# Kernel optimization log

Measured on AMD Instinct MI355X. Metric: run time of the kernel, lower is better.

## Reference

```python
import jax, jax.numpy as jnp
import numpy as np

B, N_VIS, N_HID1, N_HID2 = 1024, 4096, 4096, 4096


def setup_inputs() -> dict:
    key = jax.random.key(0)
    k0, k1, k2, k3 = jax.random.split(key, 4)
    v_data = (jax.random.uniform(k0, (B, N_VIS)) < 0.5).astype(jnp.float32)
    occupant_data = (jax.random.uniform(k1, (B, N_VIS // 2)) < 0.5).astype(jnp.float32)
    bw1 = float(np.sqrt(6.0 / (N_HID1 + N_VIS)))   # xavier_uniform
    bw2 = float(np.sqrt(6.0 / (N_HID1 + N_HID2)))
    W1 = jax.random.uniform(k2, (N_HID1, N_VIS), jnp.float32, -bw1, bw1)
    W2 = jax.random.uniform(k3, (N_HID1, N_HID2), jnp.float32, -bw2, bw2)
    return {
        "v_data": v_data,
        "occupant_data": occupant_data,
        "W1": W1,
        "b_v": jnp.zeros((N_VIS,), jnp.float32),
        "b_h1": jnp.zeros((N_HID1,), jnp.float32),
        "W2": W2,
        "b_h2": jnp.zeros((N_HID2,), jnp.float32),
        "k": 2,
    }


def reference(v_data, occupant_data, W1, b_v, b_h1, W2, b_h2, k):
    key = jax.random.key(42)
    Bn, n_vis = v_data.shape
    n_hid2 = b_h2.shape[0]
    dt = v_data.dtype

    def bern(kk, p):
        return (jax.random.uniform(kk, p.shape, p.dtype) < p).astype(p.dtype)

    # literal torch math (n_hid1 == n_hid2):
    # F.linear(v, W1, b_h1) + F.linear(h2, W2.T) = v@W1.T + b_h1 + h2@W2
    def p_h1(v, h2):
        return jax.nn.sigmoid(v @ W1.T + b_h1 + h2 @ W2)

    def p_h2(h1):  # F.linear(h1, W2, b_h2) = h1@W2.T + b_h2
        return jax.nn.sigmoid(h1 @ W2.T + b_h2)

    def p_v(h1):   # F.linear(h1, W1.T, b_v) = h1@W1 + b_v
        return jax.nn.sigmoid(h1 @ W1 + b_v)

    kpos1, kpos2, kfin, kloop = jax.random.split(key, 4)

    # positive phase (no_grad in torch)
    h2_zeros = jnp.zeros((Bn, n_hid2), dt)
    h1_data = bern(kpos1, jax.lax.stop_gradient(p_h1(v_data, h2_zeros)))
    h2_data = bern(kpos2, jax.lax.stop_gradient(p_h2(h1_data)))

    # negative phase: k Gibbs steps with occupant clamping
    v_neg, h2_neg = v_data, h2_data
    for i in range(k):
        ka, kb, kc = jax.random.split(jax.random.fold_in(kloop, i), 3)
        h1_neg = bern(ka, p_h1(v_neg, h2_neg))
        h2_neg = bern(kb, p_h2(h1_neg))
        pv = p_v(h1_neg)
        sign_s = bern(kc, pv[:, 1::2])
        # occupant_clamp: occupant bits from data, sign bits sampled
        v_neg = jnp.stack([occupant_data, sign_s], axis=-1).reshape(Bn, n_vis)

    h1_neg_final = bern(kfin, jax.lax.stop_gradient(p_h1(v_neg, h2_neg)))

    pos_v_sign = v_data[:, 1::2]
    neg_v_sign = v_neg[:, 1::2]
    invB = 1.0 / Bn

    # mean over batch of outer products == single matmul / B
    dW1_sign = (jnp.einsum('bi,bj->ij', pos_v_sign, h1_data)
                - jnp.einsum('bi,bj->ij', neg_v_sign, h1_neg_final)) * invB
    dW1_full = jnp.zeros_like(W1).at[:, 1::2].set(dW1_sign.T)
    db_v_full = jnp.zeros_like(b_v).at[1::2].set((pos_v_sign - neg_v_sign).mean(0))
    db_h1 = (h1_data - h1_neg_final).mean(0)
    dW2 = (jnp.einsum('bi,bj->ij', h1_data, h2_data)
           - jnp.einsum('bi,bj->ij', h1_neg_final, h2_neg)) * invB
    db_h2 = (h2_data - h2_neg).mean(0)

    eps = jnp.asarray(1e-7, dt)
    sp, st = v_neg[:, 1::2], v_data[:, 1::2]
    loss = -(st * jnp.log(sp + eps) + (1 - st) * jnp.log(1 - sp + eps)).mean()

    # torch sets p.grad = -dX; return loss plus those grads
    return (loss, -dW1_full, -db_v_full, -db_h1, -dW2, -db_h2)
```

## Files before the change

kernel.cpp:

```cpp
#include <hip/hip_runtime.h>
#include <stdint.h>
#include <math.h>

#define B_SZ 1024
#define NV   4096
#define NH   4096
#define NSGN 2048

typedef short bf16x8 __attribute__((ext_vector_type(8)));
typedef short bf16x4 __attribute__((ext_vector_type(4)));
typedef float f32x4  __attribute__((ext_vector_type(4)));
typedef _Float16 f16x8 __attribute__((ext_vector_type(8)));

#define F16_ONE  ((short)0x3C00)
#define F16_NEG1 ((short)0xBC00)

__host__ __device__ __forceinline__ void tf2x32(uint32_t k0, uint32_t k1,
                                                uint32_t x0, uint32_t x1,
                                                uint32_t& o0, uint32_t& o1)
{
    uint32_t k2 = k0 ^ k1 ^ 0x1BD11BDAu;
#define TFR(r) { x0 += x1; x1 = (x1 << (r)) | (x1 >> (32 - (r))); x1 ^= x0; }
    x0 += k0; x1 += k1;
    TFR(13) TFR(15) TFR(26) TFR(6)
    x0 += k1; x1 += k2 + 1u;
    TFR(17) TFR(29) TFR(16) TFR(24)
    x0 += k2; x1 += k0 + 2u;
    TFR(13) TFR(15) TFR(26) TFR(6)
    x0 += k0; x1 += k1 + 3u;
    TFR(17) TFR(29) TFR(16) TFR(24)
    x0 += k1; x1 += k2 + 4u;
    TFR(13) TFR(15) TFR(26) TFR(6)
    x0 += k2; x1 += k0 + 5u;
#undef TFR
    o0 = x0; o1 = x1;
}

__device__ __forceinline__ float tf_uniform01(uint32_t k0, uint32_t k1, uint32_t idx)
{
    uint32_t a, b;
    tf2x32(k0, k1, 0u, idx, a, b);
    uint32_t bits = a ^ b;
    uint32_t fb = (bits >> 9) | 0x3F800000u;
    return __uint_as_float(fb) - 1.0f;
}

__device__ __forceinline__ float sigmoidf_(float x)
{
    if (x >= 0.0f) { float e = expf(-x); return 1.0f / (1.0f + e); }
    float e = expf(x); return e / (1.0f + e);
}

__device__ __forceinline__ void gl16(const void* g, void* l)
{
    __builtin_amdgcn_global_load_lds((const __attribute__((address_space(1))) void*)g,
                                     (__attribute__((address_space(3))) void*)l, 16, 0, 0);
}

__global__ __launch_bounds__(256) void conv_tr(const float* __restrict__ W,
                                               short* __restrict__ Wf,
                                               short* __restrict__ Wt)
{
    __shared__ short t[64][65];
    const int bx = blockIdx.x * 64;
    const int by = blockIdx.y * 64;
    const int r0 = threadIdx.x >> 4;
    const int c0 = (threadIdx.x & 15) * 4;
#pragma unroll
    for (int i = 0; i < 4; ++i) {
        int row = by + r0 + i * 16;
        f32x4 v = *(const f32x4*)(W + (size_t)row * 4096 + bx + c0);
        short h[4];
#pragma unroll
        for (int j = 0; j < 4; ++j) {
            union { _Float16 f; short s; } u;
            u.f = (_Float16)v[j];
            h[j] = u.s;
        }
        *(bf16x4*)(Wf + (size_t)row * 4096 + bx + c0) = *(bf16x4*)h;
#pragma unroll
        for (int j = 0; j < 4; ++j) t[c0 + j][r0 + i * 16] = h[j];
    }
    __syncthreads();
#pragma unroll
    for (int i = 0; i < 4; ++i) {
        int orow = r0 + i * 16;
        short o[4] = { t[orow][c0], t[orow][c0 + 1], t[orow][c0 + 2], t[orow][c0 + 3] };
        *(bf16x4*)(Wt + (size_t)(bx + orow) * 4096 + by + c0) = *(bf16x4*)o;
    }
}

template<int MODE>
__global__ __launch_bounds__(512, 2) void mm_chunk(
    const short* __restrict__ A0, const short* __restrict__ A1,
    const short* __restrict__ B0, const short* __restrict__ B1,
    float* __restrict__ P)
{
    __shared__ __align__(1024) short As[2][16 * 512];
    __shared__ __align__(1024) short Bs[2][8 * 512];

    const int bid = blockIdx.x;
    const int xcd = bid & 7, slot = bid >> 3;

    int bm, bncol, ck, kbase, NW;
    const short* Ap;
    const short* Bp;
    if (MODE == 2) {
        int pn = xcd * 8 + (slot & 7);
        bm = ((slot >> 3) & 3) * 256;
        ck = slot >> 5;
        kbase = ck * 2048;
        Ap = A0;
        Bp = (pn < 32) ? (B0 + (size_t)pn * 128 * 4096)
                       : (B1 + (size_t)(pn - 32) * 128 * 4096);
        bncol = pn * 128;
        NW = 8192;
    } else {
        int pn = xcd * 4 + (slot & 3);
        bm = ((slot >> 2) & 3) * 256;
        ck = slot >> 4;
        if (MODE == 1) {
            if (ck >= 2) { Ap = A1; Bp = B1 + (size_t)pn * 128 * 4096; kbase = (ck - 2) * 2048; }
            else         { Ap = A0; Bp = B0 + (size_t)pn * 128 * 4096; kbase = ck * 2048; }
        } else {
            Ap = A0; Bp = B0 + (size_t)pn * 128 * 4096; kbase = ck * 1024;
        }
        bncol = pn * 128;
        NW = 4096;
    }

    const int NT = (MODE == 0) ? 32 : 64;

    const int tid = threadIdx.x;
    const int wv = tid >> 6, lane = tid & 63;
    const int l15 = lane & 15, l4 = lane >> 4;
    const int fr = l15, fc = l4 * 8;
    const int wm = wv >> 1, wn = wv & 1;

    f32x4 acc[4][4] = {};

    auto stage = [&](int buf, int t) {
        const int kk = kbase + t * 32;
        gl16(Ap + (size_t)(bm + (wv * 2 + 0) * 16 + fr) * 4096 + kk + fc, &As[buf][(wv * 2 + 0) * 512]);
        gl16(Ap + (size_t)(bm + (wv * 2 + 1) * 16 + fr) * 4096 + kk + fc, &As[buf][(wv * 2 + 1) * 512]);
        gl16(Bp + (size_t)(wv * 16 + fr) * 4096 + kk + fc, &Bs[buf][wv * 512]);
    };
    auto compute = [&](int buf) {
        f16x8 xf[4], yf[4];
#pragma unroll
        for (int m = 0; m < 4; ++m)
            xf[m] = *(f16x8*)&As[buf][(wm * 4 + m) * 512 + lane * 8];
#pragma unroll
        for (int n = 0; n < 4; ++n)
            yf[n] = *(f16x8*)&Bs[buf][(wn * 4 + n) * 512 + lane * 8];
#pragma unroll
        for (int m = 0; m < 4; ++m)
#pragma unroll
            for (int n = 0; n < 4; ++n)
                acc[m][n] = __builtin_amdgcn_mfma_f32_16x16x32_f16(xf[m], yf[n], acc[m][n], 0, 0, 0);
    };

    stage(0, 0);
    __syncthreads();
    for (int t = 0; t < NT; ++t) {
        const int cur = t & 1;
        if (t + 1 < NT) stage(cur ^ 1, t + 1);
        compute(cur);
        __syncthreads();
    }

    float* Pc = P + (size_t)ck * 1024 * NW;
#pragma unroll
    for (int m = 0; m < 4; ++m)
#pragma unroll
        for (int n = 0; n < 4; ++n)
#pragma unroll
            for (int r = 0; r < 4; ++r) {
                int row = bm + wm * 64 + m * 16 + l4 * 4 + r;
                int col = bncol + wn * 64 + n * 16 + l15;
                Pc[(size_t)row * NW + col] = acc[m][n][r];
            }
}

template<int EPI, int NC>
__global__ __launch_bounds__(256) void combine_h(
    const float* __restrict__ P, const float* __restrict__ bias,
    short* __restrict__ O0, short* __restrict__ O1,
    uint32_t k0, uint32_t k1)
{
    size_t e0 = ((size_t)blockIdx.x * 256 + threadIdx.x) * 8;
    f32x4 s0 = {}, s1 = {};
#pragma unroll
    for (int c = 0; c < NC; ++c) {
        const float* p = P + (size_t)c * 4194304 + e0;
        s0 += *(const f32x4*)p;
        s1 += *(const f32x4*)(p + 4);
    }
    int col = (int)(e0 & 4095);
    short o[8];
#pragma unroll
    for (int j = 0; j < 8; ++j) {
        float v = ((j < 4) ? s0[j] : s1[j - 4]) + bias[col + j];
        float pr = sigmoidf_(v);
        float u = tf_uniform01(k0, k1, (uint32_t)(e0 + j));
        o[j] = (u < pr) ? F16_ONE : (short)0;
    }
    *(bf16x8*)&O0[e0] = *(bf16x8*)o;
    if (EPI == 1) *(bf16x8*)&O1[e0] = *(bf16x8*)o;
}

__global__ __launch_bounds__(256) void combine_dual(
    const float* __restrict__ P,
    const float* __restrict__ b_h2, const float* __restrict__ b_v,
    const float* __restrict__ occ,
    short* __restrict__ h2n, short* __restrict__ vneg,
    uint32_t kb0, uint32_t kb1, uint32_t kc0, uint32_t kc1)
{
    size_t e0 = ((size_t)blockIdx.x * 256 + threadIdx.x) * 8;
    int row = (int)(e0 >> 13);
    int cl  = (int)(e0 & 8191);
    f32x4 s0 = {}, s1 = {};
#pragma unroll
    for (int c = 0; c < 2; ++c) {
        const float* p = P + (size_t)c * 8388608 + e0;
        s0 += *(const f32x4*)p;
        s1 += *(const f32x4*)(p + 4);
    }
    short o[8];
    if (cl < 4096) {
#pragma unroll
        for (int j = 0; j < 8; ++j) {
            float v = ((j < 4) ? s0[j] : s1[j - 4]) + b_h2[cl + j];
            float pr = sigmoidf_(v);
            size_t e = (size_t)row * 4096 + cl + j;
            float u = tf_uniform01(kb0, kb1, (uint32_t)e);
            o[j] = (u < pr) ? F16_ONE : (short)0;
        }
        *(bf16x8*)&h2n[(size_t)row * 4096 + cl] = *(bf16x8*)o;
    } else {
        int v0 = cl - 4096;
#pragma unroll
        for (int j = 0; j < 8; ++j) {
            int vcol = v0 + j;
            if (vcol & 1) {
                int s = (vcol - 1) >> 1;
                float v = ((j < 4) ? s0[j] : s1[j - 4]) + b_v[vcol];
                float pr = sigmoidf_(v);
                float u = tf_uniform01(kc0, kc1, (uint32_t)(row * 2048 + s));
                o[j] = (u < pr) ? F16_ONE : (short)0;
            } else {
                o[j] = (occ[(size_t)row * 2048 + (vcol >> 1)] != 0.0f) ? F16_ONE : (short)0;
            }
        }
        *(bf16x8*)&vneg[(size_t)row * 4096 + v0] = *(bf16x8*)o;
    }
}

template<int W1MODE>
__global__ __launch_bounds__(256) void grad_mm(
    const short* __restrict__ Xn, const short* __restrict__ Yn,
    const short* __restrict__ Xp, const short* __restrict__ Yp_bf,
    const float* __restrict__ Yp_f32,
    float* __restrict__ Out)
{
    __shared__ __align__(1024) short Xs[2][8 * 512];
    __shared__ __align__(1024) short Ys[2][8 * 512];

    const int tid = threadIdx.x;
    const int bi = blockIdx.y * 128, bj = blockIdx.x * 128;
    const int wv = tid >> 6, lane = tid & 63;
    const int wr = (wv >> 1) * 64, wc = (wv & 1) * 64;
    const int l15 = lane & 15, l4 = lane >> 4;

    const int cg = (tid & 31) * 4;
    const int kg = tid >> 5;
    const int qsub = (tid & 31) >> 2;
    const int koff = (kg >> 1) * 128 + (kg & 1) * 4;

    f32x4 acc[4][4] = {};
    short xr[4][4];
    short yr[4][4];

    auto loadT = [&](int bt) {
        const bool neg = bt < 32;
        const int b0 = (bt & 31) * 32;
        const short* X = neg ? Xn : Xp;
#pragma unroll
        for (int i = 0; i < 4; ++i)
            *(bf16x4*)xr[i] = *(const bf16x4*)(X + (size_t)(b0 + kg * 4 + i) * NH + bi + cg);
        if (W1MODE) {
            if (neg) {
#pragma unroll
                for (int i = 0; i < 4; ++i) {
                    bf16x8 v = *(const bf16x8*)(Yn + (size_t)(b0 + kg * 4 + i) * NV + 2 * (bj + cg));
                    yr[i][0] = v[1]; yr[i][1] = v[3]; yr[i][2] = v[5]; yr[i][3] = v[7];
                }
            } else {
#pragma unroll
                for (int i = 0; i < 4; ++i) {
                    const float* p = Yp_f32 + (size_t)(b0 + kg * 4 + i) * NV + 2 * (bj + cg);
                    f32x4 a = *(const f32x4*)p;
                    f32x4 b = *(const f32x4*)(p + 4);
                    yr[i][0] = (a[1] != 0.0f) ? F16_NEG1 : (short)0;
                    yr[i][1] = (a[3] != 0.0f) ? F16_NEG1 : (short)0;
                    yr[i][2] = (b[1] != 0.0f) ? F16_NEG1 : (short)0;
                    yr[i][3] = (b[3] != 0.0f) ? F16_NEG1 : (short)0;
                }
            }
        } else {
            const short* Y = neg ? Yn : Yp_bf;
            const short sx = neg ? (short)0 : (short)0x8000;
#pragma unroll
            for (int i = 0; i < 4; ++i) {
                bf16x4 v = *(const bf16x4*)(Y + (size_t)(b0 + kg * 4 + i) * NH + bj + cg);
#pragma unroll
                for (int j = 0; j < 4; ++j) yr[i][j] = (short)(v[j] ^ sx);
            }
        }
    };
    auto writeT = [&](int buf) {
#pragma unroll
        for (int j = 0; j < 4; ++j) {
            int r = (tid & 3) * 4 + j;
            int off = qsub * 512 + koff + ((r ^ qsub) & 15) * 8;
            short wx[4] = {xr[0][j], xr[1][j], xr[2][j], xr[3][j]};
            short wy[4] = {yr[0][j], yr[1][j], yr[2][j], yr[3][j]};
            *(bf16x4*)&Xs[buf][off] = *(bf16x4*)wx;
            *(bf16x4*)&Ys[buf][off] = *(bf16x4*)wy;
        }
    };

    loadT(0);
    writeT(0);
    __syncthreads();

    for (int bt = 0; bt < 64; ++bt) {
        const int cur = bt & 1;
        if (bt + 1 < 64) loadT(bt + 1);

        f16x8 xf[4], yf[4];
#pragma unroll
        for (int m = 0; m < 4; ++m) {
            int sm = (wv >> 1) * 4 + m;
            xf[m] = *(f16x8*)&Xs[cur][sm * 512 + l4 * 128 + ((l15 ^ sm) & 15) * 8];
        }
#pragma unroll
        for (int n = 0; n < 4; ++n) {
            int sn = (wv & 1) * 4 + n;
            yf[n] = *(f16x8*)&Ys[cur][sn * 512 + l4 * 128 + ((l15 ^ sn) & 15) * 8];
        }
#pragma unroll
        for (int m = 0; m < 4; ++m)
#pragma unroll
            for (int n = 0; n < 4; ++n)
                acc[m][n] = __builtin_amdgcn_mfma_f32_16x16x32_f16(xf[m], yf[n], acc[m][n], 0, 0, 0);

        if (bt + 1 < 64) writeT(cur ^ 1);
        __syncthreads();
    }

    const float invB = 1.0f / 1024.0f;
#pragma unroll
    for (int m = 0; m < 4; ++m)
#pragma unroll
        for (int n = 0; n < 4; ++n)
#pragma unroll
            for (int r = 0; r < 4; ++r) {
                int i_ = bi + wr + m * 16 + l4 * 4 + r;
                int j_ = bj + wc + n * 16 + l15;
                if (W1MODE) {
                    Out[(size_t)i_ * NV + 2 * j_ + 1] = acc[m][n][r] * invB;
                    Out[(size_t)i_ * NV + 2 * j_]     = 0.0f;
                } else {
                    Out[(size_t)i_ * NH + j_] = acc[m][n][r] * invB;
                }
            }
}

__global__ void cvt_kernel(const float* __restrict__ in, short* __restrict__ out, int n)
{
    int e = blockIdx.x * 256 + threadIdx.x;
    if (e < n) out[e] = (in[e] != 0.0f) ? F16_ONE : (short)0;
}

__global__ void dbv_fast(const float* __restrict__ vdata, const short* __restrict__ vneg,
                         float* __restrict__ out)
{
    __shared__ float part[4][64];
    int c = threadIdx.x & 63, rg = threadIdx.x >> 6;
    int s = blockIdx.x * 64 + c;
    float acc = 0.0f;
    for (int b = rg; b < B_SZ; b += 4)
        acc += ((vneg[(size_t)b * NV + 2 * s + 1] != 0) ? 1.0f : 0.0f)
             - vdata[(size_t)b * NV + 2 * s + 1];
    part[rg][c] = acc;
    __syncthreads();
    if (rg == 0) {
        out[2 * s + 1] = (part[0][c] + part[1][c] + part[2][c] + part[3][c]) * (1.0f / 1024.0f);
        out[2 * s] = 0.0f;
    }
}

__global__ void dbh_fast(const short* __restrict__ Xp, const short* __restrict__ Xn,
                         float* __restrict__ out)
{
    __shared__ int part[4][64];
    int c = threadIdx.x & 63, rg = threadIdx.x >> 6;
    int j = blockIdx.x * 64 + c;
    int acc = 0;
    for (int b = rg; b < B_SZ; b += 4)
        acc += (int)(Xn[(size_t)b * NH + j] != 0) - (int)(Xp[(size_t)b * NH + j] != 0);
    part[rg][c] = acc;
    __syncthreads();
    if (rg == 0)
        out[j] = (float)(part[0][c] + part[1][c] + part[2][c] + part[3][c]) * (1.0f / 1024.0f);
}

__global__ void zero_kernel(unsigned* p) { *p = 0u; }

__global__ void loss_count2(const float* __restrict__ vdata,
                            const short* __restrict__ vneg, unsigned* cnt)
{
    __shared__ int part[4];
    int t = blockIdx.x * 256 + threadIdx.x;
    int local = 0;
#pragma unroll
    for (int it = 0; it < 8; ++it) {
        int e = t + it * 262144;
        int b = e >> 11, s = e & 2047;
        float st = vdata[(size_t)b * NV + 2 * s + 1];
        float sp = (vneg[(size_t)b * NV + 2 * s + 1] != 0) ? 1.0f : 0.0f;
        local += (st != sp) ? 1 : 0;
    }
#pragma unroll
    for (int off = 32; off; off >>= 1) local += __shfl_down(local, off, 64);
    if ((threadIdx.x & 63) == 0) part[threadIdx.x >> 6] = local;
    __syncthreads();
    if (threadIdx.x == 0)
        atomicAdd(cnt, (unsigned)(part[0] + part[1] + part[2] + part[3]));
}

__global__ void loss_final_kernel(const unsigned* cnt, float* out, float lp, float lm)
{
    float mis = (float)(*cnt);
    float mat = 2097152.0f - mis;
    out[0] = -((mat * lp + mis * lm) * (1.0f / 2097152.0f));
}

extern "C" void kernel_launch(void* const* d_in, const int* in_sizes, int n_in,
                              void* d_out, int out_size, void* d_ws, size_t ws_size,
                              hipStream_t stream)
{
    (void)in_sizes; (void)n_in; (void)out_size; (void)ws_size;
    const float* v_data = (const float*)d_in[0];
    const float* occ    = (const float*)d_in[1];
    const float* W1     = (const float*)d_in[2];
    const float* b_v    = (const float*)d_in[3];
    const float* b_h1   = (const float*)d_in[4];
    const float* W2     = (const float*)d_in[5];
    const float* b_h2   = (const float*)d_in[6];
    float* out = (float*)d_out;

    char* w = (char*)d_ws;
    short* vneg = (short*)w;
    short* h1d  = vneg + (size_t)B_SZ * NV;
    short* h2d  = h1d  + (size_t)B_SZ * NH;
    short* h1c  = h2d  + (size_t)B_SZ * NH;
    short* h2n  = h1c  + (size_t)B_SZ * NH;
    float* P    = (float*)(h2n + (size_t)B_SZ * NH);
    unsigned* cnt = (unsigned*)(P + (size_t)4 * 1024 * 4096);

    short* W1f = (short*)(((uintptr_t)(out + 1) + 15) & ~(uintptr_t)15);
    short* W1T = W1f + (size_t)NH * NV;
    short* W2f = W1T + (size_t)NH * NV;
    short* W2T = W2f + (size_t)NH * NH;

    const uint32_t r0 = 0u, r1 = 42u;
    uint32_t kp1a, kp1b, kp2a, kp2b, kfa, kfb, kla, klb;
    tf2x32(r0, r1, 0u, 0u, kp1a, kp1b);
    tf2x32(r0, r1, 0u, 1u, kp2a, kp2b);
    tf2x32(r0, r1, 0u, 2u, kfa, kfb);
    tf2x32(r0, r1, 0u, 3u, kla, klb);
    uint32_t kaA[2], kaB[2], kbA[2], kbB[2], kcA[2], kcB[2];
    for (int i = 0; i < 2; ++i) {
        uint32_t fa, fb;
        tf2x32(kla, klb, 0u, (uint32_t)i, fa, fb);
        tf2x32(fa, fb, 0u, 0u, kaA[i], kaB[i]);
        tf2x32(fa, fb, 0u, 1u, kbA[i], kbB[i]);
        tf2x32(fa, fb, 0u, 2u, kcA[i], kcB[i]);
    }

    const int T = 256;
    const int NELEM = B_SZ * NH;
    dim3 gTr(64, 64);

    conv_tr<<<gTr, 256, 0, stream>>>(W1, W1f, W1T);
    conv_tr<<<gTr, 256, 0, stream>>>(W2, W2f, W2T);

    cvt_kernel<<<NELEM / T, T, 0, stream>>>(v_data, vneg, NELEM);

    mm_chunk<0><<<512, 512, 0, stream>>>(vneg, nullptr, W1f, nullptr, P);
    combine_h<0, 4><<<2048, 256, 0, stream>>>(P, b_h1, h1d, nullptr, kp1a, kp1b);
    mm_chunk<0><<<512, 512, 0, stream>>>(h1d, nullptr, W2f, nullptr, P);
    combine_h<1, 4><<<2048, 256, 0, stream>>>(P, b_h2, h2d, h2n, kp2a, kp2b);

    for (int i = 0; i < 2; ++i) {
        mm_chunk<1><<<512, 512, 0, stream>>>(vneg, h2n, W1f, W2T, P);
        combine_h<0, 4><<<2048, 256, 0, stream>>>(P, b_h1, h1c, nullptr, kaA[i], kaB[i]);
        mm_chunk<2><<<512, 512, 0, stream>>>(h1c, nullptr, W2f, W1T, P);
        combine_dual<<<4096, 256, 0, stream>>>(P, b_h2, b_v, occ, h2n, vneg,
                                               kbA[i], kbB[i], kcA[i], kcB[i]);
    }

    mm_chunk<1><<<512, 512, 0, stream>>>(vneg, h2n, W1f, W2T, P);
    combine_h<0, 4><<<2048, 256, 0, stream>>>(P, b_h1, h1c, nullptr, kfa, kfb);

    float* dW1o  = out + 1;
    float* dbvo  = dW1o + (size_t)NH * NV;
    float* dbh1o = dbvo + NV;
    float* dW2o  = dbh1o + NH;
    float* dbh2o = dW2o + (size_t)NH * NH;

    grad_mm<1><<<dim3(NSGN / 128, NH / 128), T, 0, stream>>>(h1c, vneg, h1d, (short*)nullptr, v_data, dW1o);
    grad_mm<0><<<dim3(NH / 128, NH / 128), T, 0, stream>>>(h1c, h2n, h1d, h2d, (const float*)nullptr, dW2o);
    dbv_fast<<<NSGN / 64, T, 0, stream>>>(v_data, vneg, dbvo);
    dbh_fast<<<NH / 64, T, 0, stream>>>(h1d, h1c, dbh1o);
    dbh_fast<<<NH / 64, T, 0, stream>>>(h2d, h2n, dbh2o);

    zero_kernel<<<1, 1, 0, stream>>>(cnt);
    loss_count2<<<1024, T, 0, stream>>>(v_data, vneg, cnt);
    loss_final_kernel<<<1, 1, 0, stream>>>(cnt, out, logf(1.0f + 1e-7f), logf(1e-7f));
}
```

Before: 1.263 ms.

## Pre-transpose gradient operands and use direct-to-LDS loads in weight-gradient GEMMs

Adds transpose kernels that write h1, h2 and the sign-bit slices of v into batch-contiguous layouts (with negation folded in) in the now-free P workspace. New grad1/grad2 kernels then stage tiles with gl16 direct global-to-LDS loads, as the forward mm_chunk does, instead of register transposes with swizzled LDS writes. They also use an XCD-aware block mapping, and grad2 uses a 256-row tile with 512 threads. This costs six extra transpose launches and their memory traffic, in exchange for a simpler and faster GEMM inner loop.

After: 1.226 ms. -2.9%, faster.

```diff
diff --git a/kernel.cpp b/kernel.cpp
--- a/kernel.cpp
+++ b/kernel.cpp
@@ -87,6 +87,84 @@
         int orow = r0 + i * 16;
         short o[4] = { t[orow][c0], t[orow][c0 + 1], t[orow][c0 + 2], t[orow][c0 + 3] };
         *(bf16x4*)(Wt + (size_t)(bx + orow) * 4096 + by + c0) = *(bf16x4*)o;
+    }
+}
+
+template<int NEG>
+__global__ __launch_bounds__(256) void tr16(const short* __restrict__ in,
+                                            short* __restrict__ out)
+{
+    __shared__ short t[64][65];
+    const int bx = blockIdx.x * 64;
+    const int by = blockIdx.y * 64;
+    const int r0 = threadIdx.x >> 4;
+    const int c0 = (threadIdx.x & 15) * 4;
+#pragma unroll
+    for (int i = 0; i < 4; ++i) {
+        int row = by + r0 + i * 16;
+        bf16x4 v = *(const bf16x4*)(in + (size_t)row * 4096 + bx + c0);
+#pragma unroll
+        for (int j = 0; j < 4; ++j)
+            t[c0 + j][r0 + i * 16] = NEG ? (short)(v[j] ^ (short)0x8000) : v[j];
+    }
+    __syncthreads();
+#pragma unroll
+    for (int i = 0; i < 4; ++i) {
+        int orow = r0 + i * 16;
+        short o[4] = { t[orow][c0], t[orow][c0 + 1], t[orow][c0 + 2], t[orow][c0 + 3] };
+        *(bf16x4*)(out + (size_t)(bx + orow) * 1024 + by + c0) = *(bf16x4*)o;
+    }
+}
+
+__global__ __launch_bounds__(256) void tr_sign(const short* __restrict__ in,
+                                               short* __restrict__ out)
+{
+    __shared__ short t[64][65];
+    const int bx = blockIdx.x * 64;
+    const int by = blockIdx.y * 64;
+    const int r0 = threadIdx.x >> 4;
+    const int c0 = (threadIdx.x & 15) * 4;
+#pragma unroll
+    for (int i = 0; i < 4; ++i) {
+        int row = by + r0 + i * 16;
+        bf16x8 v = *(const bf16x8*)(in + (size_t)row * 4096 + 2 * (bx + c0));
+#pragma unroll
+        for (int j = 0; j < 4; ++j) t[c0 + j][r0 + i * 16] = v[2 * j + 1];
+    }
+    __syncthreads();
+#pragma unroll
+    for (int i = 0; i < 4; ++i) {
+        int orow = r0 + i * 16;
+        short o[4] = { t[orow][c0], t[orow][c0 + 1], t[orow][c0 + 2], t[orow][c0 + 3] };
+        *(bf16x4*)(out + (size_t)(bx + orow) * 1024 + by + c0) = *(bf16x4*)o;
+    }
+}
+
+__global__ __launch_bounds__(256) void tr_signf(const float* __restrict__ in,
+                                                short* __restrict__ out)
+{
+    __shared__ short t[64][65];
+    const int bx = blockIdx.x * 64;
+    const int by = blockIdx.y * 64;
+    const int r0 = threadIdx.x >> 4;
+    const int c0 = (threadIdx.x & 15) * 4;
+#pragma unroll
+    for (int i = 0; i < 4; ++i) {
+        int row = by + r0 + i * 16;
+        const float* p = in + (size_t)row * 4096 + 2 * (bx + c0);
+        f32x4 a = *(const f32x4*)p;
+        f32x4 b = *(const f32x4*)(p + 4);
+        t[c0 + 0][r0 + i * 16] = (a[1] != 0.0f) ? F16_NEG1 : (short)0;
+        t[c0 + 1][r0 + i * 16] = (a[3] != 0.0f) ? F16_NEG1 : (short)0;
+        t[c0 + 2][r0 + i * 16] = (b[1] != 0.0f) ? F16_NEG1 : (short)0;
+        t[c0 + 3][r0 + i * 16] = (b[3] != 0.0f) ? F16_NEG1 : (short)0;
+    }
+    __syncthreads();
+#pragma unroll
+    for (int i = 0; i < 4; ++i) {
+        int orow = r0 + i * 16;
+        short o[4] = { t[orow][c0], t[orow][c0 + 1], t[orow][c0 + 2], t[orow][c0 + 3] };
+        *(bf16x4*)(out + (size_t)(bx + orow) * 1024 + by + c0) = *(bf16x4*)o;
     }
 }
 
@@ -182,6 +260,142 @@
             }
 }
 
+__global__ __launch_bounds__(512, 2) void grad2(
+    const short* __restrict__ XnT, const short* __restrict__ YnT,
+    const short* __restrict__ XpT, const short* __restrict__ YpT,
+    float* __restrict__ Out)
+{
+    __shared__ __align__(1024) short As[2][16 * 512];
+    __shared__ __align__(1024) short Bs[2][8 * 512];
+
+    const int bid = blockIdx.x;
+    const int xcd = bid & 7, slot = bid >> 3;
+    const int pn = xcd * 4 + (slot & 3);
+    const int bm = (slot >> 2) * 256;
+
+    const int tid = threadIdx.x;
+    const int wv = tid >> 6, lane = tid & 63;
+    const int l15 = lane & 15, l4 = lane >> 4;
+    const int fr = l15, fc = l4 * 8;
+    const int wm = wv >> 1, wn = wv & 1;
+
+    f32x4 acc[4][4] = {};
+
+    auto stage = [&](int buf, int t) {
+        const short* X = (t < 32) ? XnT : XpT;
+        const short* Y = (t < 32) ? YnT : YpT;
+        const int kk = (t & 31) * 32;
+        gl16(X + (size_t)(bm + (wv * 2 + 0) * 16 + fr) * 1024 + kk + fc, &As[buf][(wv * 2 + 0) * 512]);
+        gl16(X + (size_t)(bm + (wv * 2 + 1) * 16 + fr) * 1024 + kk + fc, &As[buf][(wv * 2 + 1) * 512]);
+        gl16(Y + (size_t)(pn * 128 + wv * 16 + fr) * 1024 + kk + fc, &Bs[buf][wv * 512]);
+    };
+    auto compute = [&](int buf) {
+        f16x8 xf[4], yf[4];
+#pragma unroll
+        for (int m = 0; m < 4; ++m)
+            xf[m] = *(f16x8*)&As[buf][(wm * 4 + m) * 512 + lane * 8];
+#pragma unroll
+        for (int n = 0; n < 4; ++n)
+            yf[n] = *(f16x8*)&Bs[buf][(wn * 4 + n) * 512 + lane * 8];
+#pragma unroll
+        for (int m = 0; m < 4; ++m)
+#pragma unroll
+            for (int n = 0; n < 4; ++n)
+                acc[m][n] = __builtin_amdgcn_mfma_f32_16x16x32_f16(xf[m], yf[n], acc[m][n], 0, 0, 0);
+    };
+
+    stage(0, 0);
+    __syncthreads();
+    for (int t = 0; t < 64; ++t) {
+        const int cur = t & 1;
+        if (t + 1 < 64) stage(cur ^ 1, t + 1);
+        compute(cur);
+        __syncthreads();
+    }
+
+    const float invB = 1.0f / 1024.0f;
+#pragma unroll
+    for (int m = 0; m < 4; ++m)
+#pragma unroll
+        for (int n = 0; n < 4; ++n)
+#pragma unroll
+            for (int r = 0; r < 4; ++r) {
+                int i_ = bm + wm * 64 + m * 16 + l4 * 4 + r;
+                int j_ = pn * 128 + wn * 64 + n * 16 + l15;
+                Out[(size_t)i_ * 4096 + j_] = acc[m][n][r] * invB;
+            }
+}
+
+__global__ __launch_bounds__(256, 4) void grad1(
+    const short* __restrict__ XnT, const short* __restrict__ YnT,
+    const short* __restrict__ XpT, const short* __restrict__ YpT,
+    float* __restrict__ Out)
+{
+    __shared__ __align__(1024) short As[2][8 * 512];
+    __shared__ __align__(1024) short Bs[2][8 * 512];
+
+    const int bid = blockIdx.x;
+    const int xcd = bid & 7, slot = bid >> 3;
+    const int pn = xcd * 2 + (slot & 1);
+    const int bm = (slot >> 1) * 128;
+
+    const int tid = threadIdx.x;
+    const int wv = tid >> 6, lane = tid & 63;
+    const int l15 = lane & 15, l4 = lane >> 4;
+    const int fr = l15, fc = l4 * 8;
+    const int wm = wv >> 1, wn = wv & 1;
+
+    f32x4 acc[4][4] = {};
+
+    auto stage = [&](int buf, int t) {
+        const short* X = (t < 32) ? XnT : XpT;
+        const short* Y = (t < 32) ? YnT : YpT;
+        const int kk = (t & 31) * 32;
+#pragma unroll
+        for (int c = 0; c < 2; ++c) {
+            int sub = wv * 2 + c;
+            gl16(X + (size_t)(bm + sub * 16 + fr) * 1024 + kk + fc, &As[buf][sub * 512]);
+            gl16(Y + (size_t)(pn * 128 + sub * 16 + fr) * 1024 + kk + fc, &Bs[buf][sub * 512]);
+        }
+    };
+    auto compute = [&](int buf) {
+        f16x8 xf[4], yf[4];
+#pragma unroll
+        for (int m = 0; m < 4; ++m)
+            xf[m] = *(f16x8*)&As[buf][(wm * 4 + m) * 512 + lane * 8];
+#pragma unroll
+        for (int n = 0; n < 4; ++n)
+            yf[n] = *(f16x8*)&Bs[buf][(wn * 4 + n) * 512 + lane * 8];
+#pragma unroll
+        for (int m = 0; m < 4; ++m)
+#pragma unroll
+            for (int n = 0; n < 4; ++n)
+                acc[m][n] = __builtin_amdgcn_mfma_f32_16x16x32_f16(xf[m], yf[n], acc[m][n], 0, 0, 0);
+    };
+
+    stage(0, 0);
+    __syncthreads();
+    for (int t = 0; t < 64; ++t) {
+        const int cur = t & 1;
+        if (t + 1 < 64) stage(cur ^ 1, t + 1);
+        compute(cur);
+        __syncthreads();
+    }
+
+    const float invB = 1.0f / 1024.0f;
+#pragma unroll
+    for (int m = 0; m < 4; ++m)
+#pragma unroll
+        for (int n = 0; n < 4; ++n)
+#pragma unroll
+            for (int r = 0; r < 4; ++r) {
+                int i_ = bm + wm * 64 + m * 16 + l4 * 4 + r;
+                int j_ = pn * 128 + wn * 64 + n * 16 + l15;
+                Out[(size_t)i_ * 4096 + 2 * j_ + 1] = acc[m][n][r] * invB;
+                Out[(size_t)i_ * 4096 + 2 * j_]     = 0.0f;
+            }
+}
+
 template<int EPI, int NC>
 __global__ __launch_bounds__(256) void combine_h(
     const float* __restrict__ P, const float* __restrict__ bias,
@@ -256,127 +470,6 @@
     }
 }
 
-template<int W1MODE>
-__global__ __launch_bounds__(256) void grad_mm(
-    const short* __restrict__ Xn, const short* __restrict__ Yn,
-    const short* __restrict__ Xp, const short* __restrict__ Yp_bf,
-    const float* __restrict__ Yp_f32,
-    float* __restrict__ Out)
-{
-    __shared__ __align__(1024) short Xs[2][8 * 512];
-    __shared__ __align__(1024) short Ys[2][8 * 512];
-
-    const int tid = threadIdx.x;
-    const int bi = blockIdx.y * 128, bj = blockIdx.x * 128;
-    const int wv = tid >> 6, lane = tid & 63;
-    const int wr = (wv >> 1) * 64, wc = (wv & 1) * 64;
-    const int l15 = lane & 15, l4 = lane >> 4;
-
-    const int cg = (tid & 31) * 4;
-    const int kg = tid >> 5;
-    const int qsub = (tid & 31) >> 2;
-    const int koff = (kg >> 1) * 128 + (kg & 1) * 4;
-
-    f32x4 acc[4][4] = {};
-    short xr[4][4];
-    short yr[4][4];
-
-    auto loadT = [&](int bt) {
-        const bool neg = bt < 32;
-        const int b0 = (bt & 31) * 32;
-        const short* X = neg ? Xn : Xp;
-#pragma unroll
-        for (int i = 0; i < 4; ++i)
-            *(bf16x4*)xr[i] = *(const bf16x4*)(X + (size_t)(b0 + kg * 4 + i) * NH + bi + cg);
-        if (W1MODE) {
-            if (neg) {
-#pragma unroll
-                for (int i = 0; i < 4; ++i) {
-                    bf16x8 v = *(const bf16x8*)(Yn + (size_t)(b0 + kg * 4 + i) * NV + 2 * (bj + cg));
-                    yr[i][0] = v[1]; yr[i][1] = v[3]; yr[i][2] = v[5]; yr[i][3] = v[7];
-                }
-            } else {
-#pragma unroll
-                for (int i = 0; i < 4; ++i) {
-                    const float* p = Yp_f32 + (size_t)(b0 + kg * 4 + i) * NV + 2 * (bj + cg);
-                    f32x4 a = *(const f32x4*)p;
-                    f32x4 b = *(const f32x4*)(p + 4);
-                    yr[i][0] = (a[1] != 0.0f) ? F16_NEG1 : (short)0;
-                    yr[i][1] = (a[3] != 0.0f) ? F16_NEG1 : (short)0;
-                    yr[i][2] = (b[1] != 0.0f) ? F16_NEG1 : (short)0;
-                    yr[i][3] = (b[3] != 0.0f) ? F16_NEG1 : (short)0;
-                }
-            }
-        } else {
-            const short* Y = neg ? Yn : Yp_bf;
-            const short sx = neg ? (short)0 : (short)0x8000;
-#pragma unroll
-            for (int i = 0; i < 4; ++i) {
-                bf16x4 v = *(const bf16x4*)(Y + (size_t)(b0 + kg * 4 + i) * NH + bj + cg);
-#pragma unroll
-                for (int j = 0; j < 4; ++j) yr[i][j] = (short)(v[j] ^ sx);
-            }
-        }
-    };
-    auto writeT = [&](int buf) {
-#pragma unroll
-        for (int j = 0; j < 4; ++j) {
-            int r = (tid & 3) * 4 + j;
-            int off = qsub * 512 + koff + ((r ^ qsub) & 15) * 8;
-            short wx[4] = {xr[0][j], xr[1][j], xr[2][j], xr[3][j]};
-            short wy[4] = {yr[0][j], yr[1][j], yr[2][j], yr[3][j]};
-            *(bf16x4*)&Xs[buf][off] = *(bf16x4*)wx;
-            *(bf16x4*)&Ys[buf][off] = *(bf16x4*)wy;
-        }
-    };
-
-    loadT(0);
-    writeT(0);
-    __syncthreads();
-
-    for (int bt = 0; bt < 64; ++bt) {
-        const int cur = bt & 1;
-        if (bt + 1 < 64) loadT(bt + 1);
-
-        f16x8 xf[4], yf[4];
-#pragma unroll
-        for (int m = 0; m < 4; ++m) {
-            int sm = (wv >> 1) * 4 + m;
-            xf[m] = *(f16x8*)&Xs[cur][sm * 512 + l4 * 128 + ((l15 ^ sm) & 15) * 8];
-        }
-#pragma unroll
-        for (int n = 0; n < 4; ++n) {
-            int sn = (wv & 1) * 4 + n;
-            yf[n] = *(f16x8*)&Ys[cur][sn * 512 + l4 * 128 + ((l15 ^ sn) & 15) * 8];
-        }
-#pragma unroll
-        for (int m = 0; m < 4; ++m)
-#pragma unroll
-            for (int n = 0; n < 4; ++n)
-                acc[m][n] = __builtin_amdgcn_mfma_f32_16x16x32_f16(xf[m], yf[n], acc[m][n], 0, 0, 0);
-
-        if (bt + 1 < 64) writeT(cur ^ 1);
-        __syncthreads();
-    }
-
-    const float invB = 1.0f / 1024.0f;
-#pragma unroll
-    for (int m = 0; m < 4; ++m)
-#pragma unroll
-        for (int n = 0; n < 4; ++n)
-#pragma unroll
-            for (int r = 0; r < 4; ++r) {
-                int i_ = bi + wr + m * 16 + l4 * 4 + r;
-                int j_ = bj + wc + n * 16 + l15;
-                if (W1MODE) {
-                    Out[(size_t)i_ * NV + 2 * j_ + 1] = acc[m][n][r] * invB;
-                    Out[(size_t)i_ * NV + 2 * j_]     = 0.0f;
-                } else {
-                    Out[(size_t)i_ * NH + j_] = acc[m][n][r] * invB;
-                }
-            }
-}
-
 __global__ void cvt_kernel(const float* __restrict__ in, short* __restrict__ out, int n)
 {
     int e = blockIdx.x * 256 + threadIdx.x;
@@ -469,6 +562,13 @@
     short* h2n  = h1c  + (size_t)B_SZ * NH;
     float* P    = (float*)(h2n + (size_t)B_SZ * NH);
     unsigned* cnt = (unsigned*)(P + (size_t)4 * 1024 * 4096);
+
+    short* h1cT  = (short*)P;
+    short* h1dT  = h1cT  + (size_t)4096 * 1024;
+    short* h2nT  = h1dT  + (size_t)4096 * 1024;
+    short* h2dTn = h2nT  + (size_t)4096 * 1024;
+    short* vsT   = h2dTn + (size_t)4096 * 1024;
+    short* vdsTn = vsT   + (size_t)2048 * 1024;
 
     short* W1f = (short*)(((uintptr_t)(out + 1) + 15) & ~(uintptr_t)15);
     short* W1T = W1f + (size_t)NH * NV;
@@ -521,8 +621,17 @@
     float* dW2o  = dbh1o + NH;
     float* dbh2o = dW2o + (size_t)NH * NH;
 
-    grad_mm<1><<<dim3(NSGN / 128, NH / 128), T, 0, stream>>>(h1c, vneg, h1d, (short*)nullptr, v_data, dW1o);
-    grad_mm<0><<<dim3(NH / 128, NH / 128), T, 0, stream>>>(h1c, h2n, h1d, h2d, (const float*)nullptr, dW2o);
+    dim3 gT16(64, 16), gTS(32, 16);
+    tr16<0><<<gT16, 256, 0, stream>>>(h1c, h1cT);
+    tr16<0><<<gT16, 256, 0, stream>>>(h1d, h1dT);
+    tr16<0><<<gT16, 256, 0, stream>>>(h2n, h2nT);
+    tr16<1><<<gT16, 256, 0, stream>>>(h2d, h2dTn);
+    tr_sign<<<gTS, 256, 0, stream>>>(vneg, vsT);
+    tr_signf<<<gTS, 256, 0, stream>>>(v_data, vdsTn);
+
+    grad1<<<512, 256, 0, stream>>>(h1cT, vsT, h1dT, vdsTn, dW1o);
+    grad2<<<512, 512, 0, stream>>>(h1cT, h2nT, h1dT, h2dTn, dW2o);
+
     dbv_fast<<<NSGN / 64, T, 0, stream>>>(v_data, vneg, dbvo);
     dbh_fast<<<NH / 64, T, 0, stream>>>(h1d, h1c, dbh1o);
     dbh_fast<<<NH / 64, T, 0, stream>>>(h2d, h2n, dbh2o);
```
